# Kernel tuning notes

Measured on AMD Instinct MI355X. Metric: run time of the kernel, lower is better.

## Reference

```python
import jax, jax.numpy as jnp
import numpy as np

BETA = 0.25  # commitment cost


def setup_inputs() -> dict:
    key = jax.random.key(0)
    k1, k2 = jax.random.split(key)
    z = jax.random.normal(k1, (16, 512, 64, 64), dtype=jnp.float32)       # (B, C=e_dim, H, W)
    codebook = jax.random.normal(k2, (1024, 512), dtype=jnp.float32)      # (n_e, e_dim)
    return {"z": z, "codebook": codebook}


def reference(z, codebook):
    b, c, h, w = z.shape
    zp = jnp.transpose(z, (0, 2, 3, 1))                                   # (B, H, W, C)
    zf = zp.reshape(-1, c)                                                # (N, e_dim)

    d = (jnp.sum(zf * zf, axis=1, keepdims=True)
         + jnp.sum(codebook * codebook, axis=1)
         - 2.0 * (zf @ codebook.T))                                       # (N, n_e)
    idx = jnp.argmin(d, axis=1)                                           # (N,)

    # one-hot @ codebook == direct gather
    z_q = codebook[idx].reshape(zp.shape)                                 # (B, H, W, C)

    sg = jax.lax.stop_gradient
    e_latent_loss = jnp.mean((sg(z_q) - zp) ** 2)
    q_latent_loss = jnp.mean((z_q - sg(zp)) ** 2)
    codebook_loss = q_latent_loss + BETA * e_latent_loss

    # straight-through estimator
    z_q_st = zp + sg(z_q - zp)
    z_q_out = jnp.transpose(z_q_st, (0, 3, 1, 2))                         # (B, C, H, W)
    return z_q_out, codebook_loss, idx.reshape(b, 1, h, w)
```

## Files before the change

### kernel.cpp

```cpp
#include <hip/hip_runtime.h>
#include <hip/hip_bf16.h>


typedef _Float16 h8 __attribute__((ext_vector_type(8)));
typedef float f32x16 __attribute__((ext_vector_type(16)));

#define OUT_LOSS  33554432
#define OUT_IDX   33554433
#define MARGIN_T  0.15f

__device__ __forceinline__ void gload_lds16(const void* g, void* l) {
  __builtin_amdgcn_global_load_lds(
      (const __attribute__((address_space(1))) void*)g,
      (__attribute__((address_space(3))) void*)l, 16, 0, 0);
}

__global__ __launch_bounds__(64) void k0_prep(
    const float* __restrict__ cb, unsigned short* __restrict__ cb16,
    float* __restrict__ cnp, int* __restrict__ counters, float* __restrict__ loss_acc,
    int* __restrict__ idx_ws, unsigned long long* __restrict__ packed_ws)
{
  const int r = blockIdx.x, l = threadIdx.x;
  const float* row = cb + (size_t)r * 512;
  float4 a  = *(const float4*)(row + l * 8);
  float4 b4 = *(const float4*)(row + l * 8 + 4);
  h8 hv;
  hv[0] = (_Float16)a.x;  hv[1] = (_Float16)a.y;  hv[2] = (_Float16)a.z;  hv[3] = (_Float16)a.w;
  hv[4] = (_Float16)b4.x; hv[5] = (_Float16)b4.y; hv[6] = (_Float16)b4.z; hv[7] = (_Float16)b4.w;
  *reinterpret_cast<h8*>(cb16 + (size_t)r * 512 + l * 8) = hv;
  float s = a.x*a.x + a.y*a.y + a.z*a.z + a.w*a.w
          + b4.x*b4.x + b4.y*b4.y + b4.z*b4.z + b4.w*b4.w;
  #pragma unroll
  for (int off = 1; off < 64; off <<= 1) s += __shfl_xor(s, off);
  if (l == 0) {
    int jr = r & 31, c = r >> 5;
    int khalf = (jr >> 2) & 1;
    int pat = jr - (khalf << 2);
    int rr2 = (pat & 3) + ((pat >> 3) << 2);
    cnp[(c << 5) + (khalf << 4) + rr2] = 0.5f * s;
  }
  const int pix = (r << 6) + l;
  idx_ws[pix] = (int)0x80000000;
  packed_ws[pix] = ~0ull;
  if (r == 0 && l == 0) { counters[0] = 0; counters[1] = 0; *loss_acc = 0.f; }
}

__global__ __launch_bounds__(256, 2) void k1_main(
    const float* __restrict__ z, const unsigned short* __restrict__ cb16,
    const float* __restrict__ cnp,
    int* __restrict__ idx_ws, int* __restrict__ flaglist,
    unsigned long long* __restrict__ pairlist, int* __restrict__ counters)
{
  extern __shared__ char smem[];
  float* cn_lds = reinterpret_cast<float*>(smem + 49152);
  const int tid   = threadIdx.x;
  const int lane  = tid & 63;
  const int wave  = tid >> 6;
  const int pxl   = lane & 31;
  const int khalf = lane >> 5;
  const int px0   = blockIdx.x << 7;
  const int b     = px0 >> 12;
  const int hw0   = px0 & 4095;
  const char* cbB = reinterpret_cast<const char*>(cb16);
  const int laneoff = pxl * 1024 + khalf * 16;

  #pragma unroll
  for (int i = 0; i < 4; ++i)
    gload_lds16(cbB + laneoff + wave * 128 + i * 32,
                smem + wave * 4096 + i * 1024);
  #pragma unroll
  for (int i = 0; i < 4; ++i)
    gload_lds16(cbB + 512 + laneoff + wave * 128 + i * 32,
                smem + 16384 + wave * 4096 + i * 1024);

  h8 bfrag[32];
  {
    const float* zl = z + ((size_t)(b * 512 + khalf * 8)) * 4096 + hw0 + (wave << 5) + pxl;
    #pragma unroll
    for (int s = 0; s < 32; ++s) {
      const float* zs = zl + (size_t)s * 16 * 4096;
      h8 hv;
      #pragma unroll
      for (int e = 0; e < 8; ++e) hv[e] = (_Float16)zs[(size_t)e * 4096];
      bfrag[s] = hv;
    }
  }
  for (int i = tid; i < 1024; i += 256) cn_lds[i] = cnp[i];
  __syncthreads();

  float v0 = INFINITY, v1 = INFINITY, v2 = INFINITY, v3 = INFINITY;
  int   i0 = 0, i1 = 0, i2 = 0, i3 = 0;
  f32x16 acca, accb;
  #pragma unroll
  for (int i = 0; i < 16; ++i) { acca[i] = 0.f; accb[i] = 0.f; }

  char* p0 = smem;
  char* p1 = smem + 16384;
  char* p2 = smem + 32768;

  for (int c = 0; c < 32; ++c) {
    const bool pf = (c < 31);

    asm volatile("s_waitcnt vmcnt(4)" ::: "memory");
    __builtin_amdgcn_s_barrier();
    __builtin_amdgcn_sched_barrier(0);
    if (pf) {
      const char* src = cbB + (c + 1) * 32768 + laneoff + wave * 128;
      #pragma unroll
      for (int i = 0; i < 4; ++i)
        gload_lds16(src + i * 32, p2 + wave * 4096 + i * 1024);
    }
    {
      const char* ab = p0 + (pxl << 4) + (khalf << 9);
      h8 f[16];
      #pragma unroll
      for (int q = 0; q < 16; ++q)
        f[q] = *reinterpret_cast<const h8*>(ab + (q << 10));
      __builtin_amdgcn_s_setprio(1);
      #pragma unroll
      for (int q = 0; q < 8; ++q) {
        acca = __builtin_amdgcn_mfma_f32_32x32x16_f16(f[q],     bfrag[q],     acca, 0, 0, 0);
        accb = __builtin_amdgcn_mfma_f32_32x32x16_f16(f[q + 8], bfrag[q + 8], accb, 0, 0, 0);
      }
      __builtin_amdgcn_s_setprio(0);
    }
    { char* t = p0; p0 = p1; p1 = p2; p2 = t; }

    if (pf) { asm volatile("s_waitcnt vmcnt(4)" ::: "memory"); }
    else    { asm volatile("s_waitcnt vmcnt(0)" ::: "memory"); }
    __builtin_amdgcn_s_barrier();
    __builtin_amdgcn_sched_barrier(0);
    if (pf) {
      const char* src = cbB + (c + 1) * 32768 + 512 + laneoff + wave * 128;
      #pragma unroll
      for (int i = 0; i < 4; ++i)
        gload_lds16(src + i * 32, p2 + wave * 4096 + i * 1024);
    }
    {
      const char* ab = p0 + (pxl << 4) + (khalf << 9);
      h8 f[16];
      #pragma unroll
      for (int q = 0; q < 16; ++q)
        f[q] = *reinterpret_cast<const h8*>(ab + (q << 10));
      __builtin_amdgcn_s_setprio(1);
      #pragma unroll
      for (int q = 0; q < 8; ++q) {
        acca = __builtin_amdgcn_mfma_f32_32x32x16_f16(f[q],     bfrag[16 + q],     acca, 0, 0, 0);
        accb = __builtin_amdgcn_mfma_f32_32x32x16_f16(f[q + 8], bfrag[24 + q],     accb, 0, 0, 0);
      }
      __builtin_amdgcn_s_setprio(0);
    }
    { char* t = p0; p0 = p1; p1 = p2; p2 = t; }

    {
      const float* cl = cn_lds + (c << 5) + (khalf << 4);
      float4 q0 = *(const float4*)(cl);     float4 q1 = *(const float4*)(cl + 4);
      float4 q2 = *(const float4*)(cl + 8); float4 q3 = *(const float4*)(cl + 12);
      const float cn[16] = {q0.x,q0.y,q0.z,q0.w, q1.x,q1.y,q1.z,q1.w,
                            q2.x,q2.y,q2.z,q2.w, q3.x,q3.y,q3.z,q3.w};
      float sc[16];
      #pragma unroll
      for (int r = 0; r < 16; ++r) sc[r] = cn[r] - (acca[r] + accb[r]);
      float mn = sc[0];
      #pragma unroll
      for (int r = 1; r < 16; ++r) mn = fminf(mn, sc[r]);
      if (__ballot(mn < v3)) {
        const int jbase = (c << 5) + (khalf << 2);
        #pragma unroll
        for (int r = 0; r < 16; ++r) {
          int j = jbase + ((r & 3) + ((r >> 2) << 3));
          float s = sc[r];
          bool c0 = s < v0, c1 = s < v1, c2 = s < v2, c3 = s < v3;
          v3 = c2 ? v2 : (c3 ? s : v3);  i3 = c2 ? i2 : (c3 ? j : i3);
          v2 = c1 ? v1 : (c2 ? s : v2);  i2 = c1 ? i1 : (c2 ? j : i2);
          v1 = c0 ? v0 : (c1 ? s : v1);  i1 = c0 ? i0 : (c1 ? j : i1);
          v0 = c0 ? s  : v0;             i0 = c0 ? j  : i0;
        }
      }
      #pragma unroll
      for (int i = 0; i < 16; ++i) { acca[i] = 0.f; accb[i] = 0.f; }
    }
  }

  {
    float ow0 = __shfl_xor(v0, 32), ow1 = __shfl_xor(v1, 32),
          ow2 = __shfl_xor(v2, 32), ow3 = __shfl_xor(v3, 32);
    int   oj0 = __shfl_xor(i0, 32), oj1 = __shfl_xor(i1, 32),
          oj2 = __shfl_xor(i2, 32), oj3 = __shfl_xor(i3, 32);
    const float ow[4] = {ow0, ow1, ow2, ow3};
    const int   oj[4] = {oj0, oj1, oj2, oj3};
    #pragma unroll
    for (int k = 0; k < 4; ++k) {
      float ov = ow[k]; int oi = oj[k];
      bool c0 = ov < v0, c1 = ov < v1, c2 = ov < v2, c3 = ov < v3;
      v3 = c2 ? v2 : (c3 ? ov : v3);  i3 = c2 ? i2 : (c3 ? oi : i3);
      v2 = c1 ? v1 : (c2 ? ov : v2);  i2 = c1 ? i1 : (c2 ? oi : i2);
      v1 = c0 ? v0 : (c1 ? ov : v1);  i1 = c0 ? i0 : (c1 ? oi : i1);
      v0 = c0 ? ov : v0;              i0 = c0 ? oi : i0;
    }
  }

  const int pix = px0 + (wave << 5) + lane;
  bool sane = (v0 == v0) && (v3 == v3) && ((unsigned)i0 < 1024u);
  bool unfl = sane && (v1 - v0 >= MARGIN_T);
  bool quad = sane && !unfl && (v3 - v0 >= MARGIN_T);
  bool qpred = (lane < 32) && quad;
  bool fpred = (lane < 32) && !unfl && !quad;
  if (lane < 32) idx_ws[pix] = unfl ? i0 : (int)0x80000000;

  unsigned long long qm = __ballot(qpred);
  if (qm) {
    int leader = __ffsll(qm) - 1;
    int base = 0;
    if (lane == leader) base = atomicAdd(&counters[1], __popcll(qm));
    base = __shfl(base, leader);
    if (qpred) {
      int pos = __popcll(qm & ((1ull << lane) - 1ull));
      pairlist[base + pos] = (unsigned long long)(unsigned)pix
          | ((unsigned long long)(unsigned)i0 << 16)
          | ((unsigned long long)(unsigned)i1 << 26)
          | ((unsigned long long)(unsigned)i2 << 36)
          | ((unsigned long long)(unsigned)i3 << 46);
    }
  }
  unsigned long long fm = __ballot(fpred);
  if (fm) {
    int leader = __ffsll(fm) - 1;
    int base = 0;
    if (lane == leader) base = atomicAdd(&counters[0], __popcll(fm));
    base = __shfl(base, leader);
    if (fpred) {
      int pos = __popcll(fm & ((1ull << lane) - 1ull));
      flaglist[base + pos] = pix;
    }
  }
}

__global__ __launch_bounds__(256) void k2a_quad(
    const float* __restrict__ z, const float* __restrict__ cb,
    const unsigned long long* __restrict__ pairlist, const int* __restrict__ counters,
    int* __restrict__ idx_ws)
{
  const int lane = threadIdx.x & 63;
  const int wid  = (blockIdx.x << 2) + (threadIdx.x >> 6);
  const int nwav = gridDim.x << 2;
  const int nf   = counters[1];
  for (int e = wid; e < nf; e += nwav) {
    unsigned long long pk = pairlist[e];
    int pix = (int)(pk & 0xFFFFull);
    int c0 = (int)((pk >> 16) & 1023ull), c1 = (int)((pk >> 26) & 1023ull);
    int c2 = (int)((pk >> 36) & 1023ull), c3 = (int)((pk >> 46) & 1023ull);
    const float* zp = z + (size_t)(pix >> 12) * 512 * 4096 + (pix & 4095);
    double s0 = 0, s1 = 0, s2 = 0, s3 = 0;
    #pragma unroll
    for (int k = 0; k < 8; ++k) {
      int c = lane + (k << 6);
      double zv2 = 2.0 * (double)zp[(size_t)c * 4096];
      double a;
      a = (double)cb[(size_t)c0 * 512 + c]; s0 = fma(a, a - zv2, s0);
      a = (double)cb[(size_t)c1 * 512 + c]; s1 = fma(a, a - zv2, s1);
      a = (double)cb[(size_t)c2 * 512 + c]; s2 = fma(a, a - zv2, s2);
      a = (double)cb[(size_t)c3 * 512 + c]; s3 = fma(a, a - zv2, s3);
    }
    #pragma unroll
    for (int off = 32; off > 0; off >>= 1) {
      s0 += __shfl_xor(s0, off); s1 += __shfl_xor(s1, off);
      s2 += __shfl_xor(s2, off); s3 += __shfl_xor(s3, off);
    }
    double bv = s0; int bi = c0;
    if (s1 < bv || (s1 == bv && c1 < bi)) { bv = s1; bi = c1; }
    if (s2 < bv || (s2 == bv && c2 < bi)) { bv = s2; bi = c2; }
    if (s3 < bv || (s3 == bv && c3 < bi)) { bv = s3; bi = c3; }
    if (lane == 0) idx_ws[pix] = bi;
  }
}

__global__ __launch_bounds__(256) void k2_rescan(
    const float* __restrict__ z, const float* __restrict__ cb,
    const int* __restrict__ flaglist, const int* __restrict__ counters,
    unsigned long long* __restrict__ packed_ws)
{
  __shared__ float zb[16][512];
  __shared__ unsigned long long best[16];
  __shared__ int pixl[16];
  const int t = threadIdx.x;
  const int nflag = counters[0];
  const int ntasks = ((nflag + 15) >> 4) << 2;
  for (int task = blockIdx.x; task < ntasks; task += gridDim.x) {
    const int g = task >> 2, q = task & 3;
    int rem = nflag - (g << 4);
    const int npx = rem < 16 ? rem : 16;
    if (t < 16) {
      best[t] = ~0ull;
      pixl[t] = (t < npx) ? flaglist[(g << 4) + t] : 0;
    }
    __syncthreads();
    for (int i = t; i < (npx << 9); i += 256) {
      int p = i >> 9, c = i & 511;
      int pix = pixl[p];
      zb[p][c] = z[((size_t)(pix >> 12) * 512 + c) * 4096 + (pix & 4095)];
    }
    __syncthreads();
    const int j = (q << 8) + t;
    const float* row = cb + (size_t)j * 512;
    double dot[16];
    #pragma unroll
    for (int p = 0; p < 16; ++p) dot[p] = 0.0;
    double cn = 0.0;
    for (int k = 0; k < 512; k += 4) {
      float4 cv = *(const float4*)(row + k);
      double c0 = cv.x, c1 = cv.y, c2 = cv.z, c3 = cv.w;
      cn = fma(c0, c0, cn); cn = fma(c1, c1, cn);
      cn = fma(c2, c2, cn); cn = fma(c3, c3, cn);
      #pragma unroll
      for (int p = 0; p < 16; ++p) {
        dot[p] = fma(c0, (double)zb[p][k + 0], dot[p]);
        dot[p] = fma(c1, (double)zb[p][k + 1], dot[p]);
        dot[p] = fma(c2, (double)zb[p][k + 2], dot[p]);
        dot[p] = fma(c3, (double)zb[p][k + 3], dot[p]);
      }
    }
    #pragma unroll
    for (int p = 0; p < 16; ++p) {
      if (p < npx) {
        double d = fma(-2.0, dot[p], cn);
        unsigned long long u = (unsigned long long)__double_as_longlong(d);
        u = (u >> 63) ? ~u : (u | 0x8000000000000000ull);
        unsigned long long pkk = (u & ~1023ull) | (unsigned long long)j;
        atomicMin(&best[p], pkk);
      }
    }
    __syncthreads();
    if (t < npx) atomicMin(&packed_ws[pixl[t]], best[t]);
    __syncthreads();
  }
}

__global__ __launch_bounds__(256) void k3_out(
    const float* __restrict__ z, const float* __restrict__ cb,
    const int* __restrict__ idx_ws, const unsigned long long* __restrict__ packed_ws,
    float* __restrict__ out, float* __restrict__ loss_acc)
{
  extern __shared__ float rows[];
  __shared__ int idxs[32];
  __shared__ float wsum[4];
  const int t = threadIdx.x;
  const int pix0 = blockIdx.x << 5;
  const int b = pix0 >> 12, hw0 = pix0 & 4095;
  if (t < 32) {
    int pix = pix0 + t;
    int v = idx_ws[pix];
    unsigned j = (v < 0) ? (unsigned)(packed_ws[pix] & 1023ull) : (unsigned)v;
    j &= 1023u;
    idxs[t] = (int)j;
    out[OUT_IDX + pix] = (float)j;
  }
  __syncthreads();
  for (int i = t; i < 32 * 128; i += 256) {
    int r = i >> 7, kq = (i & 127) << 2;
    float4 v = *(const float4*)(cb + (size_t)idxs[r] * 512 + kq);
    float* dst = rows + r * 513 + kq;
    dst[0] = v.x; dst[1] = v.y; dst[2] = v.z; dst[3] = v.w;
  }
  __syncthreads();
  const int pl = (t & 7) << 2;
  const int cg = t >> 3;
  float acc = 0.f;
  for (int c0 = 0; c0 < 512; c0 += 32) {
    int c = c0 + cg;
    size_t go = ((size_t)(b * 512 + c)) * 4096 + hw0 + pl;
    float4 zv = *(const float4*)(z + go);
    float q0 = rows[(pl + 0) * 513 + c], q1 = rows[(pl + 1) * 513 + c];
    float q2 = rows[(pl + 2) * 513 + c], q3 = rows[(pl + 3) * 513 + c];
    float d0 = q0 - zv.x, d1 = q1 - zv.y, d2 = q2 - zv.z, d3 = q3 - zv.w;
    acc = fmaf(d0, d0, acc); acc = fmaf(d1, d1, acc);
    acc = fmaf(d2, d2, acc); acc = fmaf(d3, d3, acc);
    float4 qv;
    qv.x = zv.x + d0; qv.y = zv.y + d1;
    qv.z = zv.z + d2; qv.w = zv.w + d3;
    *reinterpret_cast<float4*>(out + go) = qv;
  }
  #pragma unroll
  for (int off = 32; off > 0; off >>= 1) acc += __shfl_down(acc, off);
  if ((t & 63) == 0) wsum[t >> 6] = acc;
  __syncthreads();
  if (t == 0) atomicAdd(loss_acc, wsum[0] + wsum[1] + wsum[2] + wsum[3]);
}

__global__ void k4_loss(const float* __restrict__ loss_acc, float* __restrict__ out)
{
  if (threadIdx.x == 0 && blockIdx.x == 0)
    out[OUT_LOSS] = loss_acc[0] * (1.25f / 33554432.f);
}

extern "C" void kernel_launch(void* const* d_in, const int* in_sizes, int n_in,
                              void* d_out, int out_size, void* d_ws, size_t ws_size,
                              hipStream_t stream) {
  const float* z  = (const float*)d_in[0];
  const float* cb = (const float*)d_in[1];
  float* out = (float*)d_out;
  char* ws = (char*)d_ws;
  unsigned short*      cb16      = (unsigned short*)(ws);
  float*               cnp       = (float*)(ws + 1048576);
  int*                 idx_ws    = (int*)(ws + 1052672);
  unsigned long long*  packed_ws = (unsigned long long*)(ws + 1314816);
  int*                 flaglist  = (int*)(ws + 1839104);
  unsigned long long*  pairlist  = (unsigned long long*)(ws + 2095360);
  int*                 counters  = (int*)(ws + 2619648);
  float*               loss_acc  = (float*)(ws + 2619656);

  (void)hipFuncSetAttribute((const void*)k1_main,
        hipFuncAttributeMaxDynamicSharedMemorySize, 53248);
  (void)hipFuncSetAttribute((const void*)k3_out,
        hipFuncAttributeMaxDynamicSharedMemorySize, 65664);

  k0_prep<<<1024, 64, 0, stream>>>(cb, cb16, cnp, counters, loss_acc, idx_ws, packed_ws);
  k1_main<<<512, 256, 53248, stream>>>(z, cb16, cnp, idx_ws, flaglist, pairlist, counters);
  k2a_quad<<<1024, 256, 0, stream>>>(z, cb, pairlist, counters, idx_ws);
  k2_rescan<<<256, 256, 0, stream>>>(z, cb, flaglist, counters, packed_ws);
  k3_out<<<2048, 256, 65664, stream>>>(z, cb, idx_ws, packed_ws, out, loss_acc);
  k4_loss<<<1, 1, 0, stream>>>(loss_acc, out);
}
```

Before: 189.8 us.

## Split codebook search across two blocks per pixel tile and merge top-3 candidates

The main distance kernel now launches two blocks per 128-pixel tile, each scanning half of the codebook and keeping a top-3 instead of a top-4 list. The per-half candidates go to a workspace buffer, and a new merge kernel combines them into a global top-2 and a six-candidate exact rescore list. z is also loaded with coalesced float4 reads and transposed through swizzled LDS instead of strided scalar loads. This doubles the block count to fill the GPU better, at the cost of reading z twice, an extra kernel launch, wider pair entries and a cap on the full-rescan flag list.

New measurement: 322.4 us. 69.8% more time.

```diff
diff --git a/kernel.cpp b/kernel.cpp
--- a/kernel.cpp
+++ b/kernel.cpp
@@ -3,16 +3,29 @@
 
 
 typedef _Float16 h8 __attribute__((ext_vector_type(8)));
+typedef _Float16 h4 __attribute__((ext_vector_type(4)));
 typedef float f32x16 __attribute__((ext_vector_type(16)));
 
 #define OUT_LOSS  33554432
 #define OUT_IDX   33554433
 #define MARGIN_T  0.15f
+#define FLAG_CAP  16384
 
 __device__ __forceinline__ void gload_lds16(const void* g, void* l) {
   __builtin_amdgcn_global_load_lds(
       (const __attribute__((address_space(1))) void*)g,
       (__attribute__((address_space(3))) void*)l, 16, 0, 0);
+}
+
+__device__ __forceinline__ unsigned long long skey(float v, unsigned idx) {
+  unsigned u = __float_as_uint(v);
+  u = (u >> 31) ? ~u : (u | 0x80000000u);
+  return ((unsigned long long)u << 10) | idx;
+}
+__device__ __forceinline__ float unkey_val(unsigned long long k) {
+  unsigned su = (unsigned)(k >> 10);
+  unsigned bits = (su & 0x80000000u) ? (su & 0x7FFFFFFFu) : ~su;
+  return __uint_as_float(bits);
 }
 
 __global__ __launch_bounds__(64) void k0_prep(
@@ -42,14 +55,13 @@
   const int pix = (r << 6) + l;
   idx_ws[pix] = (int)0x80000000;
   packed_ws[pix] = ~0ull;
-  if (r == 0 && l == 0) { counters[0] = 0; counters[1] = 0; *loss_acc = 0.f; }
+  if (r == 0 && l < 4) counters[l] = 0;
+  if (r == 0 && l == 0) *loss_acc = 0.f;
 }
 
 __global__ __launch_bounds__(256, 2) void k1_main(
     const float* __restrict__ z, const unsigned short* __restrict__ cb16,
-    const float* __restrict__ cnp,
-    int* __restrict__ idx_ws, int* __restrict__ flaglist,
-    unsigned long long* __restrict__ pairlist, int* __restrict__ counters)
+    const float* __restrict__ cnp, float4* __restrict__ partial)
 {
   extern __shared__ char smem[];
   float* cn_lds = reinterpret_cast<float*>(smem + 49152);
@@ -58,64 +70,84 @@
   const int wave  = tid >> 6;
   const int pxl   = lane & 31;
   const int khalf = lane >> 5;
-  const int px0   = blockIdx.x << 7;
+  const int bid   = blockIdx.x;
+  const int pxg   = bid >> 1;
+  const int hc    = bid & 1;
+  const int px0   = pxg << 7;
   const int b     = px0 >> 12;
   const int hw0   = px0 & 4095;
-  const char* cbB = reinterpret_cast<const char*>(cb16);
+  const char* cbH = reinterpret_cast<const char*>(cb16) + hc * 524288;
   const int laneoff = pxl * 1024 + khalf * 16;
 
+  h8 bfrag[32];
+  #pragma unroll
+  for (int p = 0; p < 4; ++p) {
+    #pragma unroll
+    for (int it = 0; it < 4; ++it) {
+      const int cg  = tid >> 5;
+      const int cb4 = it * 32 + cg * 4;
+      const int pq  = (tid & 31) * 4;
+      const float* src = z + ((size_t)(b * 512 + p * 128 + cb4)) * 4096 + hw0 + pq;
+      float4 v0 = *(const float4*)(src);
+      float4 v1 = *(const float4*)(src + 4096);
+      float4 v2 = *(const float4*)(src + 8192);
+      float4 v3 = *(const float4*)(src + 12288);
+      const float* f0 = (const float*)&v0; const float* f1 = (const float*)&v1;
+      const float* f2 = (const float*)&v2; const float* f3 = (const float*)&v3;
+      #pragma unroll
+      for (int dp = 0; dp < 4; ++dp) {
+        h4 hv;
+        hv[0] = (_Float16)f0[dp]; hv[1] = (_Float16)f1[dp];
+        hv[2] = (_Float16)f2[dp]; hv[3] = (_Float16)f3[dp];
+        int row = pq + dp;
+        int a = ((row << 8) + cb4 * 2) ^ ((row & 15) << 4);
+        *reinterpret_cast<h4*>(smem + a) = hv;
+      }
+    }
+    __syncthreads();
+    {
+      const int row  = (wave << 5) + pxl;
+      const int sw   = (row & 15) << 4;
+      const int base = (row << 8) + (khalf << 4);
+      #pragma unroll
+      for (int ss = 0; ss < 8; ++ss)
+        bfrag[p * 8 + ss] = *reinterpret_cast<const h8*>(smem + ((base + (ss << 5)) ^ sw));
+    }
+    __syncthreads();
+  }
+
   #pragma unroll
   for (int i = 0; i < 4; ++i)
-    gload_lds16(cbB + laneoff + wave * 128 + i * 32,
-                smem + wave * 4096 + i * 1024);
+    gload_lds16(cbH + laneoff + wave * 128 + i * 32, smem + wave * 4096 + i * 1024);
   #pragma unroll
   for (int i = 0; i < 4; ++i)
-    gload_lds16(cbB + 512 + laneoff + wave * 128 + i * 32,
-                smem + 16384 + wave * 4096 + i * 1024);
-
-  h8 bfrag[32];
-  {
-    const float* zl = z + ((size_t)(b * 512 + khalf * 8)) * 4096 + hw0 + (wave << 5) + pxl;
-    #pragma unroll
-    for (int s = 0; s < 32; ++s) {
-      const float* zs = zl + (size_t)s * 16 * 4096;
-      h8 hv;
-      #pragma unroll
-      for (int e = 0; e < 8; ++e) hv[e] = (_Float16)zs[(size_t)e * 4096];
-      bfrag[s] = hv;
-    }
-  }
-  for (int i = tid; i < 1024; i += 256) cn_lds[i] = cnp[i];
+    gload_lds16(cbH + 512 + laneoff + wave * 128 + i * 32, smem + 16384 + wave * 4096 + i * 1024);
+  for (int i = tid; i < 512; i += 256) cn_lds[i] = cnp[hc * 512 + i];
   __syncthreads();
 
-  float v0 = INFINITY, v1 = INFINITY, v2 = INFINITY, v3 = INFINITY;
-  int   i0 = 0, i1 = 0, i2 = 0, i3 = 0;
+  float v0 = INFINITY, v1 = INFINITY, v2 = INFINITY;
+  int   i0 = 0, i1 = 0, i2 = 0;
   f32x16 acca, accb;
   #pragma unroll
   for (int i = 0; i < 16; ++i) { acca[i] = 0.f; accb[i] = 0.f; }
 
-  char* p0 = smem;
-  char* p1 = smem + 16384;
-  char* p2 = smem + 32768;
-
-  for (int c = 0; c < 32; ++c) {
-    const bool pf = (c < 31);
-
+  char* p0 = smem; char* p1 = smem + 16384; char* p2 = smem + 32768;
+
+  for (int c = 0; c < 16; ++c) {
+    const bool pf = (c < 15);
     asm volatile("s_waitcnt vmcnt(4)" ::: "memory");
     __builtin_amdgcn_s_barrier();
     __builtin_amdgcn_sched_barrier(0);
     if (pf) {
-      const char* src = cbB + (c + 1) * 32768 + laneoff + wave * 128;
-      #pragma unroll
-      for (int i = 0; i < 4; ++i)
-        gload_lds16(src + i * 32, p2 + wave * 4096 + i * 1024);
+      const char* src = cbH + (c + 1) * 32768 + laneoff + wave * 128;
+      #pragma unroll
+      for (int i = 0; i < 4; ++i) gload_lds16(src + i * 32, p2 + wave * 4096 + i * 1024);
     }
     {
       const char* ab = p0 + (pxl << 4) + (khalf << 9);
       h8 f[16];
       #pragma unroll
-      for (int q = 0; q < 16; ++q)
-        f[q] = *reinterpret_cast<const h8*>(ab + (q << 10));
+      for (int q = 0; q < 16; ++q) f[q] = *reinterpret_cast<const h8*>(ab + (q << 10));
       __builtin_amdgcn_s_setprio(1);
       #pragma unroll
       for (int q = 0; q < 8; ++q) {
@@ -125,28 +157,25 @@
       __builtin_amdgcn_s_setprio(0);
     }
     { char* t = p0; p0 = p1; p1 = p2; p2 = t; }
-
     if (pf) { asm volatile("s_waitcnt vmcnt(4)" ::: "memory"); }
     else    { asm volatile("s_waitcnt vmcnt(0)" ::: "memory"); }
     __builtin_amdgcn_s_barrier();
     __builtin_amdgcn_sched_barrier(0);
     if (pf) {
-      const char* src = cbB + (c + 1) * 32768 + 512 + laneoff + wave * 128;
-      #pragma unroll
-      for (int i = 0; i < 4; ++i)
-        gload_lds16(src + i * 32, p2 + wave * 4096 + i * 1024);
+      const char* src = cbH + (c + 1) * 32768 + 512 + laneoff + wave * 128;
+      #pragma unroll
+      for (int i = 0; i < 4; ++i) gload_lds16(src + i * 32, p2 + wave * 4096 + i * 1024);
     }
     {
       const char* ab = p0 + (pxl << 4) + (khalf << 9);
       h8 f[16];
       #pragma unroll
-      for (int q = 0; q < 16; ++q)
-        f[q] = *reinterpret_cast<const h8*>(ab + (q << 10));
+      for (int q = 0; q < 16; ++q) f[q] = *reinterpret_cast<const h8*>(ab + (q << 10));
       __builtin_amdgcn_s_setprio(1);
       #pragma unroll
       for (int q = 0; q < 8; ++q) {
-        acca = __builtin_amdgcn_mfma_f32_32x32x16_f16(f[q],     bfrag[16 + q],     acca, 0, 0, 0);
-        accb = __builtin_amdgcn_mfma_f32_32x32x16_f16(f[q + 8], bfrag[24 + q],     accb, 0, 0, 0);
+        acca = __builtin_amdgcn_mfma_f32_32x32x16_f16(f[q],     bfrag[16 + q], acca, 0, 0, 0);
+        accb = __builtin_amdgcn_mfma_f32_32x32x16_f16(f[q + 8], bfrag[24 + q], accb, 0, 0, 0);
       }
       __builtin_amdgcn_s_setprio(0);
     }
@@ -164,14 +193,13 @@
       float mn = sc[0];
       #pragma unroll
       for (int r = 1; r < 16; ++r) mn = fminf(mn, sc[r]);
-      if (__ballot(mn < v3)) {
-        const int jbase = (c << 5) + (khalf << 2);
+      if (__ballot(mn < v2)) {
+        const int jbase = hc * 512 + (c << 5) + (khalf << 2);
         #pragma unroll
         for (int r = 0; r < 16; ++r) {
           int j = jbase + ((r & 3) + ((r >> 2) << 3));
           float s = sc[r];
-          bool c0 = s < v0, c1 = s < v1, c2 = s < v2, c3 = s < v3;
-          v3 = c2 ? v2 : (c3 ? s : v3);  i3 = c2 ? i2 : (c3 ? j : i3);
+          bool c0 = s < v0, c1 = s < v1, c2 = s < v2;
           v2 = c1 ? v1 : (c2 ? s : v2);  i2 = c1 ? i1 : (c2 ? j : i2);
           v1 = c0 ? v0 : (c1 ? s : v1);  i1 = c0 ? i0 : (c1 ? j : i1);
           v0 = c0 ? s  : v0;             i0 = c0 ? j  : i0;
@@ -183,62 +211,96 @@
   }
 
   {
-    float ow0 = __shfl_xor(v0, 32), ow1 = __shfl_xor(v1, 32),
-          ow2 = __shfl_xor(v2, 32), ow3 = __shfl_xor(v3, 32);
-    int   oj0 = __shfl_xor(i0, 32), oj1 = __shfl_xor(i1, 32),
-          oj2 = __shfl_xor(i2, 32), oj3 = __shfl_xor(i3, 32);
-    const float ow[4] = {ow0, ow1, ow2, ow3};
-    const int   oj[4] = {oj0, oj1, oj2, oj3};
-    #pragma unroll
-    for (int k = 0; k < 4; ++k) {
+    float ow0 = __shfl_xor(v0, 32), ow1 = __shfl_xor(v1, 32), ow2 = __shfl_xor(v2, 32);
+    int   oj0 = __shfl_xor(i0, 32), oj1 = __shfl_xor(i1, 32), oj2 = __shfl_xor(i2, 32);
+    const float ow[3] = {ow0, ow1, ow2};
+    const int   oj[3] = {oj0, oj1, oj2};
+    #pragma unroll
+    for (int k = 0; k < 3; ++k) {
       float ov = ow[k]; int oi = oj[k];
-      bool c0 = ov < v0, c1 = ov < v1, c2 = ov < v2, c3 = ov < v3;
-      v3 = c2 ? v2 : (c3 ? ov : v3);  i3 = c2 ? i2 : (c3 ? oi : i3);
+      bool c0 = ov < v0, c1 = ov < v1, c2 = ov < v2;
       v2 = c1 ? v1 : (c2 ? ov : v2);  i2 = c1 ? i1 : (c2 ? oi : i2);
       v1 = c0 ? v0 : (c1 ? ov : v1);  i1 = c0 ? i0 : (c1 ? oi : i1);
       v0 = c0 ? ov : v0;              i0 = c0 ? oi : i0;
     }
   }
 
-  const int pix = px0 + (wave << 5) + lane;
-  bool sane = (v0 == v0) && (v3 == v3) && ((unsigned)i0 < 1024u);
-  bool unfl = sane && (v1 - v0 >= MARGIN_T);
-  bool quad = sane && !unfl && (v3 - v0 >= MARGIN_T);
-  bool qpred = (lane < 32) && quad;
-  bool fpred = (lane < 32) && !unfl && !quad;
-  if (lane < 32) idx_ws[pix] = unfl ? i0 : (int)0x80000000;
-
-  unsigned long long qm = __ballot(qpred);
+  if (lane < 32) {
+    const int pix = px0 + (wave << 5) + lane;
+    unsigned pk = (unsigned)i0 | ((unsigned)i1 << 10) | ((unsigned)i2 << 20);
+    float4 out4; out4.x = v0; out4.y = v1; out4.z = v2; out4.w = __uint_as_float(pk);
+    partial[hc * 65536 + pix] = out4;
+  }
+}
+
+struct ull2 { unsigned long long lo, hi; };
+__global__ __launch_bounds__(256) void k1_merge(
+    const float4* __restrict__ partial,
+    int* __restrict__ idx_ws, int* __restrict__ flaglist,
+    ull2* __restrict__ pairlist, int* __restrict__ counters)
+{
+  const int pix  = blockIdx.x * 256 + threadIdx.x;
+  const int lane = threadIdx.x & 63;
+  float4 A = partial[pix], B = partial[65536 + pix];
+  unsigned pa = __float_as_uint(A.w), pb = __float_as_uint(B.w);
+  unsigned ia0 = pa & 1023u, ia1 = (pa >> 10) & 1023u, ia2 = (pa >> 20) & 1023u;
+  unsigned ib0 = pb & 1023u, ib1 = (pb >> 10) & 1023u, ib2 = (pb >> 20) & 1023u;
+  unsigned long long k0 = skey(A.x, ia0), k1 = skey(A.y, ia1), k2 = skey(A.z, ia2);
+  unsigned long long k3 = skey(B.x, ib0), k4 = skey(B.y, ib1), k5 = skey(B.z, ib2);
+  unsigned long long m0 = k0;
+  m0 = k1 < m0 ? k1 : m0; m0 = k2 < m0 ? k2 : m0;
+  m0 = k3 < m0 ? k3 : m0; m0 = k4 < m0 ? k4 : m0; m0 = k5 < m0 ? k5 : m0;
+  unsigned long long m1 = ~0ull;
+  unsigned long long t;
+  t = (k0 == m0) ? ~0ull : k0; m1 = t < m1 ? t : m1;
+  t = (k1 == m0) ? ~0ull : k1; m1 = t < m1 ? t : m1;
+  t = (k2 == m0) ? ~0ull : k2; m1 = t < m1 ? t : m1;
+  t = (k3 == m0) ? ~0ull : k3; m1 = t < m1 ? t : m1;
+  t = (k4 == m0) ? ~0ull : k4; m1 = t < m1 ? t : m1;
+  t = (k5 == m0) ? ~0ull : k5; m1 = t < m1 ? t : m1;
+  float w0 = unkey_val(m0), w1 = unkey_val(m1);
+  int   i0 = (int)(m0 & 1023ull);
+  float cert = fminf(A.z, B.z);
+  bool sane = (w0 == w0) && (w1 == w1) && (cert == cert);
+  bool unfl = sane && (w1 - w0 >= MARGIN_T);
+  bool hex  = sane && !unfl && (cert - w0 >= MARGIN_T);
+  bool full = !unfl && !hex;
+  idx_ws[pix] = unfl ? i0 : (int)0x80000000;
+
+  unsigned long long qm = __ballot(hex);
   if (qm) {
     int leader = __ffsll(qm) - 1;
     int base = 0;
     if (lane == leader) base = atomicAdd(&counters[1], __popcll(qm));
     base = __shfl(base, leader);
-    if (qpred) {
+    if (hex) {
       int pos = __popcll(qm & ((1ull << lane) - 1ull));
-      pairlist[base + pos] = (unsigned long long)(unsigned)pix
-          | ((unsigned long long)(unsigned)i0 << 16)
-          | ((unsigned long long)(unsigned)i1 << 26)
-          | ((unsigned long long)(unsigned)i2 << 36)
-          | ((unsigned long long)(unsigned)i3 << 46);
-    }
-  }
-  unsigned long long fm = __ballot(fpred);
+      ull2 e;
+      e.lo = (unsigned long long)(unsigned)pix
+           | ((unsigned long long)ia0 << 32) | ((unsigned long long)ia1 << 42)
+           | ((unsigned long long)ia2 << 52);
+      e.hi = (unsigned long long)ib0 | ((unsigned long long)ib1 << 10)
+           | ((unsigned long long)ib2 << 20);
+      pairlist[base + pos] = e;
+    }
+  }
+  unsigned long long fm = __ballot(full);
   if (fm) {
     int leader = __ffsll(fm) - 1;
     int base = 0;
     if (lane == leader) base = atomicAdd(&counters[0], __popcll(fm));
     base = __shfl(base, leader);
-    if (fpred) {
+    if (full) {
       int pos = __popcll(fm & ((1ull << lane) - 1ull));
-      flaglist[base + pos] = pix;
-    }
-  }
-}
-
-__global__ __launch_bounds__(256) void k2a_quad(
+      int wi = base + pos;
+      if (wi < FLAG_CAP) flaglist[wi] = pix;
+    }
+  }
+}
+
+__global__ __launch_bounds__(256) void k2a_hex(
     const float* __restrict__ z, const float* __restrict__ cb,
-    const unsigned long long* __restrict__ pairlist, const int* __restrict__ counters,
+    const ull2* __restrict__ pairlist, const int* __restrict__ counters,
     int* __restrict__ idx_ws)
 {
   const int lane = threadIdx.x & 63;
@@ -246,12 +308,14 @@
   const int nwav = gridDim.x << 2;
   const int nf   = counters[1];
   for (int e = wid; e < nf; e += nwav) {
-    unsigned long long pk = pairlist[e];
-    int pix = (int)(pk & 0xFFFFull);
-    int c0 = (int)((pk >> 16) & 1023ull), c1 = (int)((pk >> 26) & 1023ull);
-    int c2 = (int)((pk >> 36) & 1023ull), c3 = (int)((pk >> 46) & 1023ull);
+    ull2 pk = pairlist[e];
+    int pix = (int)(pk.lo & 0xFFFFFFFFull);
+    int c0 = (int)((pk.lo >> 32) & 1023ull), c1 = (int)((pk.lo >> 42) & 1023ull);
+    int c2 = (int)((pk.lo >> 52) & 1023ull);
+    int c3 = (int)(pk.hi & 1023ull), c4 = (int)((pk.hi >> 10) & 1023ull);
+    int c5 = (int)((pk.hi >> 20) & 1023ull);
     const float* zp = z + (size_t)(pix >> 12) * 512 * 4096 + (pix & 4095);
-    double s0 = 0, s1 = 0, s2 = 0, s3 = 0;
+    double s0 = 0, s1 = 0, s2 = 0, s3 = 0, s4 = 0, s5 = 0;
     #pragma unroll
     for (int k = 0; k < 8; ++k) {
       int c = lane + (k << 6);
@@ -261,16 +325,21 @@
       a = (double)cb[(size_t)c1 * 512 + c]; s1 = fma(a, a - zv2, s1);
       a = (double)cb[(size_t)c2 * 512 + c]; s2 = fma(a, a - zv2, s2);
       a = (double)cb[(size_t)c3 * 512 + c]; s3 = fma(a, a - zv2, s3);
+      a = (double)cb[(size_t)c4 * 512 + c]; s4 = fma(a, a - zv2, s4);
+      a = (double)cb[(size_t)c5 * 512 + c]; s5 = fma(a, a - zv2, s5);
     }
     #pragma unroll
     for (int off = 32; off > 0; off >>= 1) {
       s0 += __shfl_xor(s0, off); s1 += __shfl_xor(s1, off);
       s2 += __shfl_xor(s2, off); s3 += __shfl_xor(s3, off);
+      s4 += __shfl_xor(s4, off); s5 += __shfl_xor(s5, off);
     }
     double bv = s0; int bi = c0;
     if (s1 < bv || (s1 == bv && c1 < bi)) { bv = s1; bi = c1; }
     if (s2 < bv || (s2 == bv && c2 < bi)) { bv = s2; bi = c2; }
     if (s3 < bv || (s3 == bv && c3 < bi)) { bv = s3; bi = c3; }
+    if (s4 < bv || (s4 == bv && c4 < bi)) { bv = s4; bi = c4; }
+    if (s5 < bv || (s5 == bv && c5 < bi)) { bv = s5; bi = c5; }
     if (lane == 0) idx_ws[pix] = bi;
   }
 }
@@ -284,7 +353,8 @@
   __shared__ unsigned long long best[16];
   __shared__ int pixl[16];
   const int t = threadIdx.x;
-  const int nflag = counters[0];
+  int nflag = counters[0];
+  if (nflag > FLAG_CAP) nflag = FLAG_CAP;
   const int ntasks = ((nflag + 15) >> 4) << 2;
   for (int task = blockIdx.x; task < ntasks; task += gridDim.x) {
     const int g = task >> 2, q = task & 3;
@@ -401,22 +471,24 @@
   float* out = (float*)d_out;
   char* ws = (char*)d_ws;
   unsigned short*      cb16      = (unsigned short*)(ws);
-  float*               cnp       = (float*)(ws + 1048576);
-  int*                 idx_ws    = (int*)(ws + 1052672);
-  unsigned long long*  packed_ws = (unsigned long long*)(ws + 1314816);
-  int*                 flaglist  = (int*)(ws + 1839104);
-  unsigned long long*  pairlist  = (unsigned long long*)(ws + 2095360);
-  int*                 counters  = (int*)(ws + 2619648);
-  float*               loss_acc  = (float*)(ws + 2619656);
+  ull2*                pairlist  = (ull2*)(ws);
+  float4*              partial   = (float4*)(ws + 1048576);
+  int*                 idx_ws    = (int*)(ws + 3145728);
+  unsigned long long*  packed_ws = (unsigned long long*)(ws + 3407872);
+  int*                 flaglist  = (int*)(ws + 3932160);
+  float*               cnp       = (float*)(ws + 3997696);
+  int*                 counters  = (int*)(ws + 4001792);
+  float*               loss_acc  = (float*)(ws + 4001856);
 
   (void)hipFuncSetAttribute((const void*)k1_main,
-        hipFuncAttributeMaxDynamicSharedMemorySize, 53248);
+        hipFuncAttributeMaxDynamicSharedMemorySize, 51200);
   (void)hipFuncSetAttribute((const void*)k3_out,
         hipFuncAttributeMaxDynamicSharedMemorySize, 65664);
 
   k0_prep<<<1024, 64, 0, stream>>>(cb, cb16, cnp, counters, loss_acc, idx_ws, packed_ws);
-  k1_main<<<512, 256, 53248, stream>>>(z, cb16, cnp, idx_ws, flaglist, pairlist, counters);
-  k2a_quad<<<1024, 256, 0, stream>>>(z, cb, pairlist, counters, idx_ws);
+  k1_main<<<1024, 256, 51200, stream>>>(z, cb16, cnp, partial);
+  k1_merge<<<256, 256, 0, stream>>>(partial, idx_ws, flaglist, pairlist, counters);
+  k2a_hex<<<1024, 256, 0, stream>>>(z, cb, pairlist, counters, idx_ws);
   k2_rescan<<<256, 256, 0, stream>>>(z, cb, flaglist, counters, packed_ws);
   k3_out<<<2048, 256, 65664, stream>>>(z, cb, idx_ws, packed_ws, out, loss_acc);
   k4_loss<<<1, 1, 0, stream>>>(loss_acc, out);
```

## Pre-tile codebook for contiguous LDS loads and stage z through swizzled LDS

Applied to the files above, without the earlier changes.

The prep kernel now writes the fp16 codebook in a tiled order that matches the LDS layout, so each thread's global-to-LDS copy reads contiguous 16-byte chunks (tid*16) rather than strided rows. The main kernel's z fragment load is rewritten to read float4 vectors coalesced across pixels, convert them to fp16 and transpose through an XOR-swizzled LDS buffer in four passes, replacing the scalar strided per-element gathers. This is meant to cut uncoalesced global traffic in the z load prologue and the codebook stream, at the cost of extra barriers and LDS round-trips before the main loop. The counter and loss accumulator workspace offsets are also adjusted.

Result: faster. 177.9 us (-6.3%).

```diff
diff --git a/kernel.cpp b/kernel.cpp
--- a/kernel.cpp
+++ b/kernel.cpp
@@ -15,8 +15,12 @@
       (__attribute__((address_space(3))) void*)l, 16, 0, 0);
 }
 
+__device__ __forceinline__ int zswz(int row) {
+  return ((row & 3) << 6) | (((row >> 2) & 3) << 4);
+}
+
 __global__ __launch_bounds__(64) void k0_prep(
-    const float* __restrict__ cb, unsigned short* __restrict__ cb16,
+    const float* __restrict__ cb, unsigned short* __restrict__ cbT,
     float* __restrict__ cnp, int* __restrict__ counters, float* __restrict__ loss_acc,
     int* __restrict__ idx_ws, unsigned long long* __restrict__ packed_ws)
 {
@@ -27,7 +31,14 @@
   h8 hv;
   hv[0] = (_Float16)a.x;  hv[1] = (_Float16)a.y;  hv[2] = (_Float16)a.z;  hv[3] = (_Float16)a.w;
   hv[4] = (_Float16)b4.x; hv[5] = (_Float16)b4.y; hv[6] = (_Float16)b4.z; hv[7] = (_Float16)b4.w;
-  *reinterpret_cast<h8*>(cb16 + (size_t)r * 512 + l * 8) = hv;
+  {
+    const int c  = r >> 5, rr = r & 31;
+    const int s  = l >> 1;
+    const int hk = l & 1;
+    char* dst = reinterpret_cast<char*>(cbT)
+              + (size_t)(c * 32 + s) * 1024 + (hk * 32 + rr) * 16;
+    *reinterpret_cast<h8*>(dst) = hv;
+  }
   float s = a.x*a.x + a.y*a.y + a.z*a.z + a.w*a.w
           + b4.x*b4.x + b4.y*b4.y + b4.z*b4.z + b4.w*b4.w;
   #pragma unroll
@@ -42,11 +53,12 @@
   const int pix = (r << 6) + l;
   idx_ws[pix] = (int)0x80000000;
   packed_ws[pix] = ~0ull;
-  if (r == 0 && l == 0) { counters[0] = 0; counters[1] = 0; *loss_acc = 0.f; }
+  if (r == 0 && l < 4) counters[l] = 0;
+  if (r == 0 && l == 0) *loss_acc = 0.f;
 }
 
 __global__ __launch_bounds__(256, 2) void k1_main(
-    const float* __restrict__ z, const unsigned short* __restrict__ cb16,
+    const float* __restrict__ z, const unsigned short* __restrict__ cbT,
     const float* __restrict__ cnp,
     int* __restrict__ idx_ws, int* __restrict__ flaglist,
     unsigned long long* __restrict__ pairlist, int* __restrict__ counters)
@@ -61,31 +73,51 @@
   const int px0   = blockIdx.x << 7;
   const int b     = px0 >> 12;
   const int hw0   = px0 & 4095;
-  const char* cbB = reinterpret_cast<const char*>(cb16);
-  const int laneoff = pxl * 1024 + khalf * 16;
+  const char* cbB = reinterpret_cast<const char*>(cbT);
+
+  h8 bfrag[32];
+  for (int i = tid; i < 1024; i += 256) cn_lds[i] = cnp[i];
+  #pragma unroll
+  for (int p = 0; p < 4; ++p) {
+    #pragma unroll
+    for (int it2 = 0; it2 < 2; ++it2) {
+      const int cg  = tid >> 5;
+      const int ch0 = it2 * 64 + cg * 8;
+      const int pq  = (tid & 31) * 4;
+      const float* src = z + ((size_t)(b * 512 + p * 128 + ch0)) * 4096 + hw0 + pq;
+      float4 v[8];
+      #pragma unroll
+      for (int j = 0; j < 8; ++j) v[j] = *(const float4*)(src + (size_t)j * 4096);
+      const float* vf = reinterpret_cast<const float*>(v);
+      #pragma unroll
+      for (int dp = 0; dp < 4; ++dp) {
+        h8 hv;
+        #pragma unroll
+        for (int j = 0; j < 8; ++j) hv[j] = (_Float16)vf[j * 4 + dp];
+        int row = pq + dp;
+        int a = (row << 8) + ch0 * 2;
+        a ^= zswz(row);
+        *reinterpret_cast<h8*>(smem + a) = hv;
+      }
+    }
+    __syncthreads();
+    {
+      const int row  = (wave << 5) + pxl;
+      const int sw   = zswz(row);
+      const int base = (row << 8) + (khalf << 4);
+      #pragma unroll
+      for (int ss = 0; ss < 8; ++ss)
+        bfrag[p * 8 + ss] = *reinterpret_cast<const h8*>(smem + ((base + (ss << 5)) ^ sw));
+    }
+    __syncthreads();
+  }
 
   #pragma unroll
   for (int i = 0; i < 4; ++i)
-    gload_lds16(cbB + laneoff + wave * 128 + i * 32,
-                smem + wave * 4096 + i * 1024);
+    gload_lds16(cbB + tid * 16 + i * 4096, smem + tid * 16 + i * 4096);
   #pragma unroll
   for (int i = 0; i < 4; ++i)
-    gload_lds16(cbB + 512 + laneoff + wave * 128 + i * 32,
-                smem + 16384 + wave * 4096 + i * 1024);
-
-  h8 bfrag[32];
-  {
-    const float* zl = z + ((size_t)(b * 512 + khalf * 8)) * 4096 + hw0 + (wave << 5) + pxl;
-    #pragma unroll
-    for (int s = 0; s < 32; ++s) {
-      const float* zs = zl + (size_t)s * 16 * 4096;
-      h8 hv;
-      #pragma unroll
-      for (int e = 0; e < 8; ++e) hv[e] = (_Float16)zs[(size_t)e * 4096];
-      bfrag[s] = hv;
-    }
-  }
-  for (int i = tid; i < 1024; i += 256) cn_lds[i] = cnp[i];
+    gload_lds16(cbB + 16384 + tid * 16 + i * 4096, smem + 16384 + tid * 16 + i * 4096);
   __syncthreads();
 
   float v0 = INFINITY, v1 = INFINITY, v2 = INFINITY, v3 = INFINITY;
@@ -100,22 +132,20 @@
 
   for (int c = 0; c < 32; ++c) {
     const bool pf = (c < 31);
-
     asm volatile("s_waitcnt vmcnt(4)" ::: "memory");
     __builtin_amdgcn_s_barrier();
     __builtin_amdgcn_sched_barrier(0);
     if (pf) {
-      const char* src = cbB + (c + 1) * 32768 + laneoff + wave * 128;
+      const char* src = cbB + (c + 1) * 32768 + tid * 16;
       #pragma unroll
       for (int i = 0; i < 4; ++i)
-        gload_lds16(src + i * 32, p2 + wave * 4096 + i * 1024);
+        gload_lds16(src + i * 4096, p2 + tid * 16 + i * 4096);
     }
     {
-      const char* ab = p0 + (pxl << 4) + (khalf << 9);
+      const char* ab = p0 + (khalf << 9) + (pxl << 4);
       h8 f[16];
       #pragma unroll
-      for (int q = 0; q < 16; ++q)
-        f[q] = *reinterpret_cast<const h8*>(ab + (q << 10));
+      for (int q = 0; q < 16; ++q) f[q] = *reinterpret_cast<const h8*>(ab + (q << 10));
       __builtin_amdgcn_s_setprio(1);
       #pragma unroll
       for (int q = 0; q < 8; ++q) {
@@ -125,28 +155,26 @@
       __builtin_amdgcn_s_setprio(0);
     }
     { char* t = p0; p0 = p1; p1 = p2; p2 = t; }
-
     if (pf) { asm volatile("s_waitcnt vmcnt(4)" ::: "memory"); }
     else    { asm volatile("s_waitcnt vmcnt(0)" ::: "memory"); }
     __builtin_amdgcn_s_barrier();
     __builtin_amdgcn_sched_barrier(0);
     if (pf) {
-      const char* src = cbB + (c + 1) * 32768 + 512 + laneoff + wave * 128;
+      const char* src = cbB + (c + 1) * 32768 + 16384 + tid * 16;
       #pragma unroll
       for (int i = 0; i < 4; ++i)
-        gload_lds16(src + i * 32, p2 + wave * 4096 + i * 1024);
+        gload_lds16(src + i * 4096, p2 + tid * 16 + i * 4096);
     }
     {
-      const char* ab = p0 + (pxl << 4) + (khalf << 9);
+      const char* ab = p0 + (khalf << 9) + (pxl << 4);
       h8 f[16];
       #pragma unroll
-      for (int q = 0; q < 16; ++q)
-        f[q] = *reinterpret_cast<const h8*>(ab + (q << 10));
+      for (int q = 0; q < 16; ++q) f[q] = *reinterpret_cast<const h8*>(ab + (q << 10));
       __builtin_amdgcn_s_setprio(1);
       #pragma unroll
       for (int q = 0; q < 8; ++q) {
-        acca = __builtin_amdgcn_mfma_f32_32x32x16_f16(f[q],     bfrag[16 + q],     acca, 0, 0, 0);
-        accb = __builtin_amdgcn_mfma_f32_32x32x16_f16(f[q + 8], bfrag[24 + q],     accb, 0, 0, 0);
+        acca = __builtin_amdgcn_mfma_f32_32x32x16_f16(f[q],     bfrag[16 + q], acca, 0, 0, 0);
+        accb = __builtin_amdgcn_mfma_f32_32x32x16_f16(f[q + 8], bfrag[24 + q], accb, 0, 0, 0);
       }
       __builtin_amdgcn_s_setprio(0);
     }
@@ -400,22 +428,22 @@
   const float* cb = (const float*)d_in[1];
   float* out = (float*)d_out;
   char* ws = (char*)d_ws;
-  unsigned short*      cb16      = (unsigned short*)(ws);
+  unsigned short*      cbT       = (unsigned short*)(ws);
   float*               cnp       = (float*)(ws + 1048576);
   int*                 idx_ws    = (int*)(ws + 1052672);
   unsigned long long*  packed_ws = (unsigned long long*)(ws + 1314816);
   int*                 flaglist  = (int*)(ws + 1839104);
   unsigned long long*  pairlist  = (unsigned long long*)(ws + 2095360);
   int*                 counters  = (int*)(ws + 2619648);
-  float*               loss_acc  = (float*)(ws + 2619656);
+  float*               loss_acc  = (float*)(ws + 2619712);
 
   (void)hipFuncSetAttribute((const void*)k1_main,
         hipFuncAttributeMaxDynamicSharedMemorySize, 53248);
   (void)hipFuncSetAttribute((const void*)k3_out,
         hipFuncAttributeMaxDynamicSharedMemorySize, 65664);
 
-  k0_prep<<<1024, 64, 0, stream>>>(cb, cb16, cnp, counters, loss_acc, idx_ws, packed_ws);
-  k1_main<<<512, 256, 53248, stream>>>(z, cb16, cnp, idx_ws, flaglist, pairlist, counters);
+  k0_prep<<<1024, 64, 0, stream>>>(cb, cbT, cnp, counters, loss_acc, idx_ws, packed_ws);
+  k1_main<<<512, 256, 53248, stream>>>(z, cbT, cnp, idx_ws, flaglist, pairlist, counters);
   k2a_quad<<<1024, 256, 0, stream>>>(z, cb, pairlist, counters, idx_ws);
   k2_rescan<<<256, 256, 0, stream>>>(z, cb, flaglist, counters, packed_ws);
   k3_out<<<2048, 256, 65664, stream>>>(z, cb, idx_ws, packed_ws, out, loss_acc);
```
